# Kernel optimization log

Measured on AMD Instinct MI355X. Metric: run time of the kernel, lower is better.

The kernel has to match this reference:

```python
import jax, jax.numpy as jnp
import numpy as np

N_NODES = 50000
N_EDGES = 800000
NODE_DIM = 128
EDGE_DIM = 64
HIDDEN = 128
OUT_DIM = 64


def graph_conv(x, W, b, src, dst, num_segments):
    # h = linear(x); out[dst] += h[src]  (scatter-add / segment-sum aggregation)
    h = x @ W + b
    return jax.ops.segment_sum(h[src], dst, num_segments=num_segments)


def setup_inputs() -> dict:
    key = jax.random.key(0)
    ks = jax.random.split(key, 12)
    s = 1.0 / np.sqrt(HIDDEN)
    return {
        "node_features": jax.random.normal(ks[0], (N_NODES, NODE_DIM), dtype=jnp.float32),
        "edge_index": jax.random.randint(ks[1], (2, N_EDGES), 0, N_NODES, dtype=jnp.int64),
        "edge_features": jax.random.normal(ks[2], (N_EDGES, EDGE_DIM), dtype=jnp.float32),
        "edge_meta_index": jax.random.randint(ks[3], (2, N_EDGES), 0, N_EDGES, dtype=jnp.int64),
        "W1": jax.random.normal(ks[4], (NODE_DIM, HIDDEN), dtype=jnp.float32) * s,
        "b1": jnp.zeros((HIDDEN,), dtype=jnp.float32),
        "W2": jax.random.normal(ks[5], (HIDDEN, HIDDEN), dtype=jnp.float32) * s,
        "b2": jnp.zeros((HIDDEN,), dtype=jnp.float32),
        "We": jax.random.normal(ks[6], (EDGE_DIM, HIDDEN), dtype=jnp.float32) * s,
        "be": jnp.zeros((HIDDEN,), dtype=jnp.float32),
        "Wfc": jax.random.normal(ks[7], (2 * HIDDEN, OUT_DIM), dtype=jnp.float32) * s,
        "bfc": jnp.zeros((OUT_DIM,), dtype=jnp.float32),
    }


def reference(node_features, edge_index, edge_features, edge_meta_index,
              W1, b1, W2, b2, We, be, Wfc, bfc):
    row, col = edge_index[0], edge_index[1]
    mrow, mcol = edge_meta_index[0], edge_meta_index[1]

    # two node GraphConvs (dropout is identity in eval / p=0)
    x = jax.nn.relu(graph_conv(node_features, W1, b1, row, col, N_NODES))
    x = jax.nn.relu(graph_conv(x, W2, b2, row, col, N_NODES))

    # edge GraphConv on the line graph: e has one row per original edge
    e = graph_conv(edge_features, We, be, mrow, mcol, N_EDGES)

    # per-edge scatter-add aggregation (vectorized form of the Python loop):
    # aggregated_neighbors[dest] += x[src]; aggregated_edges[dest] += e[idx]
    agg_neighbors = jax.ops.segment_sum(x[row], col, num_segments=N_NODES)
    agg_edges = jax.ops.segment_sum(e, col, num_segments=N_NODES)

    out = jnp.concatenate([x + agg_neighbors, agg_edges], axis=1) @ Wfc + bfc
    return out
```

## Files before the change

kernel.cpp:

```cpp
#include <hip/hip_runtime.h>

#define N_NODES 50000
#define N_EDGES 800000
#define NODE_DIM 128
#define EDGE_DIM 64
#define HIDDEN 128
#define OUT_DIM 64

#define NBKT 196
#define CAP 4864
#define EPB 4096
#define NBLK1 196

typedef unsigned short u16;
typedef unsigned int u32;
typedef __attribute__((ext_vector_type(8))) short bf16x8;
typedef __attribute__((ext_vector_type(4))) float f32x4;

__device__ __forceinline__ float bflo(u32 u) { return __builtin_bit_cast(float, u << 16); }
__device__ __forceinline__ float bfhi(u32 u) { return __builtin_bit_cast(float, u & 0xFFFF0000u); }
__device__ __forceinline__ u32 pack2(float x, float y) {
    u32 a = __builtin_bit_cast(u32, x);
    a += 0x7FFFu + ((a >> 16) & 1u);
    u32 b = __builtin_bit_cast(u32, y);
    b += 0x7FFFu + ((b >> 16) & 1u);
    return (a >> 16) | (b & 0xFFFF0000u);
}
__device__ __forceinline__ u16 bf16r(float x) {
    u32 a = __builtin_bit_cast(u32, x);
    a += 0x7FFFu + ((a >> 16) & 1u);
    return (u16)(a >> 16);
}

__global__ __launch_bounds__(256) void pre1(
    const float* __restrict__ We, const float* __restrict__ be,
    const float* __restrict__ Wfc, const float* __restrict__ W1,
    const float* __restrict__ W2,
    float* __restrict__ Wcomb, float* __restrict__ bvec,
    short* __restrict__ W1t, short* __restrict__ W2t,
    int* __restrict__ bcur, int* __restrict__ bcurm)
{
    int idx = blockIdx.x * 256 + threadIdx.x;
    if (idx < 4096) {
        int k = idx >> 6, c = idx & 63;
        float s = 0.f;
        for (int h = 0; h < 128; h++)
            s = fmaf(We[k * 128 + h], Wfc[(128 + h) * 64 + c], s);
        Wcomb[idx] = s;
    } else if (idx < 4160) {
        int c = idx - 4096;
        float s = 0.f;
        for (int h = 0; h < 128; h++)
            s = fmaf(be[h], Wfc[(128 + h) * 64 + c], s);
        bvec[c] = s;
    } else if (idx < 20544) {
        int i = idx - 4160; int n = i >> 7, k = i & 127;
        W1t[n * 128 + k] = (short)bf16r(W1[k * 128 + n]);
    } else if (idx < 36928) {
        int i = idx - 20544; int n = i >> 7, k = i & 127;
        W2t[n * 128 + k] = (short)bf16r(W2[k * 128 + n]);
    } else if (idx < 37320) {
        int i = idx - 36928;
        if (i < 196) bcur[i] = i * CAP;
        else bcurm[i - 196] = (i - 196) * CAP;
    }
}

__global__ __launch_bounds__(256) void pre2(
    const float* __restrict__ Wfc, const float* __restrict__ Wcomb,
    short* __restrict__ Wft)
{
    int idx = blockIdx.x * 256 + threadIdx.x;
    if (idx < 64 * 192) {
        int n = idx / 192, k = idx - n * 192;
        float v = (k < 128) ? Wfc[k * 64 + n] : Wcomb[(k - 128) * 64 + n];
        Wft[n * 192 + k] = (short)bf16r(v);
    }
}

__global__ __launch_bounds__(256) void bin_pairs(
    const int* __restrict__ row, const int* __restrict__ col,
    const int* __restrict__ mrow, const int* __restrict__ mcol,
    int* __restrict__ bcur, int* __restrict__ bcurm,
    u32* __restrict__ pairs, u32* __restrict__ pairsm)
{
    int prob = (blockIdx.x >= NBLK1) ? 1 : 0;
    int blk = blockIdx.x - prob * NBLK1;
    int base = blk * EPB;
    int t = threadIdx.x;
    __shared__ int lh[NBKT];
    __shared__ int lbase[NBKT];
    __shared__ int lcur[NBKT];
    for (int i = t; i < NBKT; i += 256) { lh[i] = 0; lcur[i] = 0; }
    __syncthreads();
    int k[16], v[16];
    #pragma unroll
    for (int i = 0; i < 16; i++) {
        int idx = base + i * 256 + t;
        if (idx < N_EDGES) {
            if (!prob) { k[i] = col[idx]; v[i] = row[idx]; }
            else       { k[i] = col[mcol[idx]]; v[i] = mrow[idx]; }
            atomicAdd(&lh[k[i] >> 8], 1);
        } else {
            k[i] = -1; v[i] = 0;
        }
    }
    __syncthreads();
    int* gcur = prob ? bcurm : bcur;
    for (int i = t; i < NBKT; i += 256)
        lbase[i] = atomicAdd(&gcur[i], lh[i]);
    __syncthreads();
    u32* PR = prob ? pairsm : pairs;
    #pragma unroll
    for (int i = 0; i < 16; i++) {
        if (k[i] >= 0) {
            int bk = k[i] >> 8;
            int p = lbase[bk] + atomicAdd(&lcur[bk], 1);
            if (p < (bk + 1) * CAP)
                PR[p] = (u32)v[i] | ((u32)(k[i] & 255) << 24);
        }
    }
}

__global__ __launch_bounds__(256) void bucket_fill(
    const u32* __restrict__ pairs, const u32* __restrict__ pairsm,
    const int* __restrict__ bcur, const int* __restrict__ bcurm,
    int* __restrict__ offp, int* __restrict__ deg, int* __restrict__ ids,
    int* __restrict__ offpm, int* __restrict__ degm, int* __restrict__ idsm)
{
    int prob = (blockIdx.x >= NBKT) ? 1 : 0;
    int b = blockIdx.x - prob * NBKT;
    const u32* PR = prob ? pairsm : pairs;
    int cnt_total = (prob ? bcurm[b] : bcur[b]) - b * CAP;
    if (cnt_total > CAP) cnt_total = CAP;
    int n0 = b << 8;
    int nn = N_NODES - n0; if (nn > 256) nn = 256;
    __shared__ int hist[256];
    __shared__ int cur[256];
    __shared__ int wsum[4];
    __shared__ u32 pbuf[CAP];
    int t = threadIdx.x;
    hist[t] = 0;
    __syncthreads();
    for (int i = t; i < cnt_total; i += 256) {
        u32 pr = PR[(size_t)b * CAP + i];
        pbuf[i] = pr;
        atomicAdd(&hist[pr >> 24], 1);
    }
    __syncthreads();
    int h = hist[t];
    int x = h;
    int lane = t & 63, wid = t >> 6;
    for (int d = 1; d < 64; d <<= 1) {
        int u = __shfl_up(x, d, 64);
        if (lane >= d) x += u;
    }
    if (lane == 63) wsum[wid] = x;
    __syncthreads();
    int wex = 0;
    for (int i = 0; i < wid; i++) wex += wsum[i];
    int excl = wex + x - h;
    cur[t] = excl;
    if (t < nn) {
        if (!prob) { offp[n0 + t] = b * CAP + excl; deg[n0 + t] = h; }
        else       { offpm[n0 + t] = b * CAP + excl; degm[n0 + t] = h; }
    }
    __syncthreads();
    int* OI = prob ? idsm : ids;
    for (int i = t; i < cnt_total; i += 256) {
        u32 pr = pbuf[i];
        int p = atomicAdd(&cur[pr >> 24], 1);
        OI[(size_t)b * CAP + p] = (int)(pr & 0xFFFFFFu);
    }
}

__global__ __launch_bounds__(256) void gemm_mfma_f32(
    const float* __restrict__ A, const short* __restrict__ Wt,
    u16* __restrict__ P, int M)
{
    __shared__ short As[64 * 128];
    __shared__ short Ws[128 * 128];
    int t = threadIdx.x;
    int r0 = blockIdx.x * 64;
    for (int i = t; i < 64 * 32; i += 256) {
        int row = i >> 5, c4 = i & 31;
        int gr = r0 + row;
        float4 v = make_float4(0.f, 0.f, 0.f, 0.f);
        if (gr < M) v = ((const float4*)(A + (size_t)gr * 128))[c4];
        uint2 u; u.x = pack2(v.x, v.y); u.y = pack2(v.z, v.w);
        *(uint2*)((char*)As + row * 256 + ((c4 * 8) ^ ((row & 7) << 4))) = u;
    }
    for (int i = t; i < 128 * 16; i += 256) {
        int row = i >> 4, c16 = i & 15;
        uint4 u = *(const uint4*)((const char*)Wt + row * 256 + c16 * 16);
        *(uint4*)((char*)Ws + row * 256 + ((c16 * 16) ^ ((row & 7) << 4))) = u;
    }
    __syncthreads();
    int w = t >> 6, l = t & 63, lr = l & 15, q = l >> 4;
    int rh = (w & 1) * 32, ch = (w >> 1) * 64;
    f32x4 acc[2][4];
    #pragma unroll
    for (int rt = 0; rt < 2; rt++)
        #pragma unroll
        for (int ct = 0; ct < 4; ct++) acc[rt][ct] = (f32x4){0.f, 0.f, 0.f, 0.f};
    #pragma unroll
    for (int kk = 0; kk < 4; kk++) {
        int bo = kk * 64 + q * 16;
        bf16x8 a[2];
        #pragma unroll
        for (int rt = 0; rt < 2; rt++) {
            int ar = rh + rt * 16 + lr;
            a[rt] = *(const bf16x8*)((const char*)As + ar * 256 + (bo ^ ((ar & 7) << 4)));
        }
        #pragma unroll
        for (int ct = 0; ct < 4; ct++) {
            int br = ch + ct * 16 + lr;
            bf16x8 b = *(const bf16x8*)((const char*)Ws + br * 256 + (bo ^ ((br & 7) << 4)));
            acc[0][ct] = __builtin_amdgcn_mfma_f32_16x16x32_bf16(a[0], b, acc[0][ct], 0, 0, 0);
            acc[1][ct] = __builtin_amdgcn_mfma_f32_16x16x32_bf16(a[1], b, acc[1][ct], 0, 0, 0);
        }
    }
    #pragma unroll
    for (int rt = 0; rt < 2; rt++)
        #pragma unroll
        for (int reg = 0; reg < 4; reg++) {
            int gr = r0 + rh + rt * 16 + q * 4 + reg;
            if (gr < M) {
                #pragma unroll
                for (int ct = 0; ct < 4; ct++)
                    P[(size_t)gr * 128 + ch + ct * 16 + lr] = bf16r(acc[rt][ct][reg]);
            }
        }
}

__global__ __launch_bounds__(256) void gemm_mfma_bf16(
    const u16* __restrict__ A, const short* __restrict__ Wt,
    u16* __restrict__ P, int M)
{
    __shared__ short As[64 * 128];
    __shared__ short Ws[128 * 128];
    int t = threadIdx.x;
    int r0 = blockIdx.x * 64;
    for (int i = t; i < 64 * 16; i += 256) {
        int row = i >> 4, c16 = i & 15;
        int gr = r0 + row;
        uint4 u = make_uint4(0u, 0u, 0u, 0u);
        if (gr < M) u = *(const uint4*)((const char*)A + (size_t)gr * 256 + c16 * 16);
        *(uint4*)((char*)As + row * 256 + ((c16 * 16) ^ ((row & 7) << 4))) = u;
    }
    for (int i = t; i < 128 * 16; i += 256) {
        int row = i >> 4, c16 = i & 15;
        uint4 u = *(const uint4*)((const char*)Wt + row * 256 + c16 * 16);
        *(uint4*)((char*)Ws + row * 256 + ((c16 * 16) ^ ((row & 7) << 4))) = u;
    }
    __syncthreads();
    int w = t >> 6, l = t & 63, lr = l & 15, q = l >> 4;
    int rh = (w & 1) * 32, ch = (w >> 1) * 64;
    f32x4 acc[2][4];
    #pragma unroll
    for (int rt = 0; rt < 2; rt++)
        #pragma unroll
        for (int ct = 0; ct < 4; ct++) acc[rt][ct] = (f32x4){0.f, 0.f, 0.f, 0.f};
    #pragma unroll
    for (int kk = 0; kk < 4; kk++) {
        int bo = kk * 64 + q * 16;
        bf16x8 a[2];
        #pragma unroll
        for (int rt = 0; rt < 2; rt++) {
            int ar = rh + rt * 16 + lr;
            a[rt] = *(const bf16x8*)((const char*)As + ar * 256 + (bo ^ ((ar & 7) << 4)));
        }
        #pragma unroll
        for (int ct = 0; ct < 4; ct++) {
            int br = ch + ct * 16 + lr;
            bf16x8 b = *(const bf16x8*)((const char*)Ws + br * 256 + (bo ^ ((br & 7) << 4)));
            acc[0][ct] = __builtin_amdgcn_mfma_f32_16x16x32_bf16(a[0], b, acc[0][ct], 0, 0, 0);
            acc[1][ct] = __builtin_amdgcn_mfma_f32_16x16x32_bf16(a[1], b, acc[1][ct], 0, 0, 0);
        }
    }
    #pragma unroll
    for (int rt = 0; rt < 2; rt++)
        #pragma unroll
        for (int reg = 0; reg < 4; reg++) {
            int gr = r0 + rh + rt * 16 + q * 4 + reg;
            if (gr < M) {
                #pragma unroll
                for (int ct = 0; ct < 4; ct++)
                    P[(size_t)gr * 128 + ch + ct * 16 + lr] = bf16r(acc[rt][ct][reg]);
            }
        }
}

__global__ __launch_bounds__(256) void agg_relu_q(
    const u16* __restrict__ P, const int* __restrict__ offp,
    const int* __restrict__ deg,
    const int* __restrict__ ids, const float* __restrict__ bias,
    u16* __restrict__ X, int M)
{
    int qid = threadIdx.x >> 4;
    int l = threadIdx.x & 15;
    int w = blockIdx.x * 16 + qid;
    if (w >= M) return;
    int beg = offp[w], end = beg + deg[w];
    const uint4* F = (const uint4*)P;
    float a0 = 0.f, a1 = 0.f, a2 = 0.f, a3 = 0.f,
          a4 = 0.f, a5 = 0.f, a6 = 0.f, a7 = 0.f;
    int i = beg;
    for (; i + 3 < end; i += 4) {
        uint4 v0 = F[(size_t)ids[i]     * 16 + l];
        uint4 v1 = F[(size_t)ids[i + 1] * 16 + l];
        uint4 v2 = F[(size_t)ids[i + 2] * 16 + l];
        uint4 v3 = F[(size_t)ids[i + 3] * 16 + l];
        a0 += bflo(v0.x) + bflo(v1.x) + bflo(v2.x) + bflo(v3.x);
        a1 += bfhi(v0.x) + bfhi(v1.x) + bfhi(v2.x) + bfhi(v3.x);
        a2 += bflo(v0.y) + bflo(v1.y) + bflo(v2.y) + bflo(v3.y);
        a3 += bfhi(v0.y) + bfhi(v1.y) + bfhi(v2.y) + bfhi(v3.y);
        a4 += bflo(v0.z) + bflo(v1.z) + bflo(v2.z) + bflo(v3.z);
        a5 += bfhi(v0.z) + bfhi(v1.z) + bfhi(v2.z) + bfhi(v3.z);
        a6 += bflo(v0.w) + bflo(v1.w) + bflo(v2.w) + bflo(v3.w);
        a7 += bfhi(v0.w) + bfhi(v1.w) + bfhi(v2.w) + bfhi(v3.w);
    }
    for (; i < end; i++) {
        uint4 v = F[(size_t)ids[i] * 16 + l];
        a0 += bflo(v.x); a1 += bfhi(v.x);
        a2 += bflo(v.y); a3 += bfhi(v.y);
        a4 += bflo(v.z); a5 += bfhi(v.z);
        a6 += bflo(v.w); a7 += bfhi(v.w);
    }
    float dg = (float)(end - beg);
    float4 b0 = ((const float4*)bias)[2 * l];
    float4 b1 = ((const float4*)bias)[2 * l + 1];
    a0 = fmaxf(fmaf(dg, b0.x, a0), 0.f);
    a1 = fmaxf(fmaf(dg, b0.y, a1), 0.f);
    a2 = fmaxf(fmaf(dg, b0.z, a2), 0.f);
    a3 = fmaxf(fmaf(dg, b0.w, a3), 0.f);
    a4 = fmaxf(fmaf(dg, b1.x, a4), 0.f);
    a5 = fmaxf(fmaf(dg, b1.y, a5), 0.f);
    a6 = fmaxf(fmaf(dg, b1.z, a6), 0.f);
    a7 = fmaxf(fmaf(dg, b1.w, a7), 0.f);
    uint4 o;
    o.x = pack2(a0, a1); o.y = pack2(a2, a3);
    o.z = pack2(a4, a5); o.w = pack2(a6, a7);
    ((uint4*)(X + (size_t)w * 128))[l] = o;
}

__global__ __launch_bounds__(256) void agg_epilogue_q(
    const u16* __restrict__ X2, const float* __restrict__ ef,
    const int* __restrict__ offp, const int* __restrict__ deg,
    const int* __restrict__ ids,
    const int* __restrict__ offpm, const int* __restrict__ degm,
    const int* __restrict__ mids,
    u16* __restrict__ S, u16* __restrict__ Gg, int M)
{
    int qid = threadIdx.x >> 4;
    int l = threadIdx.x & 15;
    int w = blockIdx.x * 16 + qid;
    if (w >= M) return;
    {
        int beg = offp[w], end = beg + deg[w];
        const uint4* F = (const uint4*)X2;
        uint4 own = F[(size_t)w * 16 + l];
        float a0 = bflo(own.x), a1 = bfhi(own.x),
              a2 = bflo(own.y), a3 = bfhi(own.y),
              a4 = bflo(own.z), a5 = bfhi(own.z),
              a6 = bflo(own.w), a7 = bfhi(own.w);
        int i = beg;
        for (; i + 3 < end; i += 4) {
            uint4 v0 = F[(size_t)ids[i]     * 16 + l];
            uint4 v1 = F[(size_t)ids[i + 1] * 16 + l];
            uint4 v2 = F[(size_t)ids[i + 2] * 16 + l];
            uint4 v3 = F[(size_t)ids[i + 3] * 16 + l];
            a0 += bflo(v0.x) + bflo(v1.x) + bflo(v2.x) + bflo(v3.x);
            a1 += bfhi(v0.x) + bfhi(v1.x) + bfhi(v2.x) + bfhi(v3.x);
            a2 += bflo(v0.y) + bflo(v1.y) + bflo(v2.y) + bflo(v3.y);
            a3 += bfhi(v0.y) + bfhi(v1.y) + bfhi(v2.y) + bfhi(v3.y);
            a4 += bflo(v0.z) + bflo(v1.z) + bflo(v2.z) + bflo(v3.z);
            a5 += bfhi(v0.z) + bfhi(v1.z) + bfhi(v2.z) + bfhi(v3.z);
            a6 += bflo(v0.w) + bflo(v1.w) + bflo(v2.w) + bflo(v3.w);
            a7 += bfhi(v0.w) + bfhi(v1.w) + bfhi(v2.w) + bfhi(v3.w);
        }
        for (; i < end; i++) {
            uint4 v = F[(size_t)ids[i] * 16 + l];
            a0 += bflo(v.x); a1 += bfhi(v.x);
            a2 += bflo(v.y); a3 += bfhi(v.y);
            a4 += bflo(v.z); a5 += bfhi(v.z);
            a6 += bflo(v.w); a7 += bfhi(v.w);
        }
        uint4 o;
        o.x = pack2(a0, a1); o.y = pack2(a2, a3);
        o.z = pack2(a4, a5); o.w = pack2(a6, a7);
        ((uint4*)(S + (size_t)w * 128))[l] = o;
    }
    {
        int beg = offpm[w], end = beg + degm[w];
        const float4* E = (const float4*)ef;
        float g0 = 0.f, g1 = 0.f, g2 = 0.f, g3 = 0.f;
        int i = beg;
        for (; i + 3 < end; i += 4) {
            float4 v0 = E[(size_t)mids[i]     * 16 + l];
            float4 v1 = E[(size_t)mids[i + 1] * 16 + l];
            float4 v2 = E[(size_t)mids[i + 2] * 16 + l];
            float4 v3 = E[(size_t)mids[i + 3] * 16 + l];
            g0 += v0.x + v1.x + v2.x + v3.x;
            g1 += v0.y + v1.y + v2.y + v3.y;
            g2 += v0.z + v1.z + v2.z + v3.z;
            g3 += v0.w + v1.w + v2.w + v3.w;
        }
        for (; i < end; i++) {
            float4 v = E[(size_t)mids[i] * 16 + l];
            g0 += v.x; g1 += v.y; g2 += v.z; g3 += v.w;
        }
        uint2 o;
        o.x = pack2(g0, g1); o.y = pack2(g2, g3);
        ((uint2*)(Gg + (size_t)w * 64))[l] = o;
    }
}

__global__ __launch_bounds__(256) void final_mfma(
    const u16* __restrict__ S, const u16* __restrict__ Gg,
    const int* __restrict__ degm, const short* __restrict__ Wft,
    const float* __restrict__ bvec, const float* __restrict__ bfc,
    float* __restrict__ out, int M)
{
    __shared__ short As[64 * 192];
    __shared__ short Ws[64 * 192];
    int t = threadIdx.x;
    int r0 = blockIdx.x * 64;
    for (int i = t; i < 64 * 16; i += 256) {
        int row = i >> 4, c16 = i & 15;
        int gr = r0 + row;
        uint4 u = make_uint4(0u, 0u, 0u, 0u);
        if (gr < M) u = *(const uint4*)((const char*)S + (size_t)gr * 256 + c16 * 16);
        *(uint4*)((char*)As + row * 384 + ((c16 * 16) ^ ((row & 7) << 4))) = u;
    }
    for (int i = t; i < 64 * 8; i += 256) {
        int row = i >> 3, c16 = i & 7;
        int gr = r0 + row;
        uint4 u = make_uint4(0u, 0u, 0u, 0u);
        if (gr < M) u = *(const uint4*)((const char*)Gg + (size_t)gr * 128 + c16 * 16);
        *(uint4*)((char*)As + row * 384 + ((256 + c16 * 16) ^ ((row & 7) << 4))) = u;
    }
    for (int i = t; i < 64 * 24; i += 256) {
        int row = i / 24, c16 = i - row * 24;
        uint4 u = *(const uint4*)((const char*)Wft + row * 384 + c16 * 16);
        *(uint4*)((char*)Ws + row * 384 + ((c16 * 16) ^ ((row & 7) << 4))) = u;
    }
    __syncthreads();
    int w = t >> 6, l = t & 63, lr = l & 15, q = l >> 4;
    int rh = (w & 1) * 32, ch = (w >> 1) * 32;
    f32x4 acc[2][2];
    #pragma unroll
    for (int rt = 0; rt < 2; rt++)
        #pragma unroll
        for (int ct = 0; ct < 2; ct++) acc[rt][ct] = (f32x4){0.f, 0.f, 0.f, 0.f};
    #pragma unroll
    for (int kk = 0; kk < 6; kk++) {
        int bo = kk * 64 + q * 16;
        bf16x8 a[2];
        #pragma unroll
        for (int rt = 0; rt < 2; rt++) {
            int ar = rh + rt * 16 + lr;
            a[rt] = *(const bf16x8*)((const char*)As + ar * 384 + (bo ^ ((ar & 7) << 4)));
        }
        #pragma unroll
        for (int ct = 0; ct < 2; ct++) {
            int br = ch + ct * 16 + lr;
            bf16x8 b = *(const bf16x8*)((const char*)Ws + br * 384 + (bo ^ ((br & 7) << 4)));
            acc[0][ct] = __builtin_amdgcn_mfma_f32_16x16x32_bf16(a[0], b, acc[0][ct], 0, 0, 0);
            acc[1][ct] = __builtin_amdgcn_mfma_f32_16x16x32_bf16(a[1], b, acc[1][ct], 0, 0, 0);
        }
    }
    float bv0 = bvec[ch + lr], bv1 = bvec[ch + 16 + lr];
    float bf0 = bfc[ch + lr],  bf1 = bfc[ch + 16 + lr];
    #pragma unroll
    for (int rt = 0; rt < 2; rt++)
        #pragma unroll
        for (int reg = 0; reg < 4; reg++) {
            int gr = r0 + rh + rt * 16 + q * 4 + reg;
            if (gr < M) {
                float cnt = (float)degm[gr];
                out[(size_t)gr * 64 + ch + lr]      = acc[rt][0][reg] + fmaf(cnt, bv0, bf0);
                out[(size_t)gr * 64 + ch + 16 + lr] = acc[rt][1][reg] + fmaf(cnt, bv1, bf1);
            }
        }
}

extern "C" void kernel_launch(void* const* d_in, const int* in_sizes, int n_in,
                              void* d_out, int out_size, void* d_ws, size_t ws_size,
                              hipStream_t stream)
{
    const float* nf  = (const float*)d_in[0];
    const int*   ei  = (const int*)d_in[1];
    const float* ef  = (const float*)d_in[2];
    const int*   emi = (const int*)d_in[3];
    const float* W1  = (const float*)d_in[4];
    const float* b1  = (const float*)d_in[5];
    const float* W2  = (const float*)d_in[6];
    const float* b2  = (const float*)d_in[7];
    const float* We  = (const float*)d_in[8];
    const float* be  = (const float*)d_in[9];
    const float* Wfc = (const float*)d_in[10];
    const float* bfc = (const float*)d_in[11];

    const int* row  = ei;
    const int* col  = ei + N_EDGES;
    const int* mrow = emi;
    const int* mcol = emi + N_EDGES;

    u16* A  = (u16*)d_ws;
    u16* B  = A + (size_t)N_NODES * 128;
    u16* S  = B + (size_t)N_NODES * 128;
    u16* Gg = S + (size_t)N_NODES * 128;
    u32* pairs  = (u32*)(Gg + (size_t)N_NODES * 64);
    u32* pairsm = pairs + (size_t)NBKT * CAP;
    float* Wcomb = (float*)(pairsm + (size_t)NBKT * CAP);
    float* bvec  = Wcomb + 64 * 64;
    short* W1t = (short*)(bvec + 64);
    short* W2t = W1t + 128 * 128;
    short* Wft = W2t + 128 * 128;
    int* offp  = (int*)(Wft + 64 * 192);
    int* deg   = offp + N_NODES;
    int* offpm = deg + N_NODES;
    int* degm  = offpm + N_NODES;
    int* bcur  = degm + N_NODES;
    int* bcurm = bcur + 256;
    int* ids   = bcurm + 256;
    int* idsm  = ids + (size_t)NBKT * CAP;

    pre1<<<146, 256, 0, stream>>>(We, be, Wfc, W1, W2, Wcomb, bvec, W1t, W2t, bcur, bcurm);

    bin_pairs<<<2 * NBLK1, 256, 0, stream>>>(row, col, mrow, mcol,
                                             bcur, bcurm, pairs, pairsm);
    bucket_fill<<<2 * NBKT, 256, 0, stream>>>(pairs, pairsm, bcur, bcurm,
                                              offp, deg, ids, offpm, degm, idsm);
    pre2<<<48, 256, 0, stream>>>(Wfc, Wcomb, Wft);

    gemm_mfma_f32<<<(N_NODES + 63) / 64, 256, 0, stream>>>(nf, W1t, A, N_NODES);
    agg_relu_q<<<(N_NODES + 15) / 16, 256, 0, stream>>>(A, offp, deg, ids, b1, B, N_NODES);
    gemm_mfma_bf16<<<(N_NODES + 63) / 64, 256, 0, stream>>>(B, W2t, A, N_NODES);
    agg_relu_q<<<(N_NODES + 15) / 16, 256, 0, stream>>>(A, offp, deg, ids, b2, B, N_NODES);
    agg_epilogue_q<<<(N_NODES + 15) / 16, 256, 0, stream>>>(
        B, ef, offp, deg, ids, offpm, degm, idsm, S, Gg, N_NODES);
    final_mfma<<<(N_NODES + 63) / 64, 256, 0, stream>>>(
        S, Gg, degm, Wft, bvec, bfc, (float*)d_out, N_NODES);
}
```

Baseline: 482.1 us.

## Split node features into column slices for cache-resident gathers

```diff
diff --git a/kernel.cpp b/kernel.cpp
--- a/kernel.cpp
+++ b/kernel.cpp
@@ -11,6 +11,10 @@
 #define CAP 4864
 #define EPB 4096
 #define NBLK1 196
+
+#define NSLC 4
+#define SLC_STRIDE ((size_t)N_NODES * 32)
+#define NBN 782
 
 typedef unsigned short u16;
 typedef unsigned int u32;
@@ -227,8 +231,11 @@
             int gr = r0 + rh + rt * 16 + q * 4 + reg;
             if (gr < M) {
                 #pragma unroll
-                for (int ct = 0; ct < 4; ct++)
-                    P[(size_t)gr * 128 + ch + ct * 16 + lr] = bf16r(acc[rt][ct][reg]);
+                for (int ct = 0; ct < 4; ct++) {
+                    int cb = ch + ct * 16;
+                    P[(size_t)(cb >> 5) * SLC_STRIDE + (size_t)gr * 32 + (cb & 31) + lr]
+                        = bf16r(acc[rt][ct][reg]);
+                }
             }
         }
 }
@@ -245,7 +252,8 @@
         int row = i >> 4, c16 = i & 15;
         int gr = r0 + row;
         uint4 u = make_uint4(0u, 0u, 0u, 0u);
-        if (gr < M) u = *(const uint4*)((const char*)A + (size_t)gr * 256 + c16 * 16);
+        if (gr < M)
+            u = ((const uint4*)(A + (size_t)(c16 >> 2) * SLC_STRIDE + (size_t)gr * 32))[c16 & 3];
         *(uint4*)((char*)As + row * 256 + ((c16 * 16) ^ ((row & 7) << 4))) = u;
     }
     for (int i = t; i < 128 * 16; i += 256) {
@@ -285,32 +293,37 @@
             int gr = r0 + rh + rt * 16 + q * 4 + reg;
             if (gr < M) {
                 #pragma unroll
-                for (int ct = 0; ct < 4; ct++)
-                    P[(size_t)gr * 128 + ch + ct * 16 + lr] = bf16r(acc[rt][ct][reg]);
+                for (int ct = 0; ct < 4; ct++) {
+                    int cb = ch + ct * 16;
+                    P[(size_t)(cb >> 5) * SLC_STRIDE + (size_t)gr * 32 + (cb & 31) + lr]
+                        = bf16r(acc[rt][ct][reg]);
+                }
             }
         }
 }
 
-__global__ __launch_bounds__(256) void agg_relu_q(
+__global__ __launch_bounds__(256) void agg_relu_s(
     const u16* __restrict__ P, const int* __restrict__ offp,
     const int* __restrict__ deg,
     const int* __restrict__ ids, const float* __restrict__ bias,
     u16* __restrict__ X, int M)
 {
-    int qid = threadIdx.x >> 4;
-    int l = threadIdx.x & 15;
-    int w = blockIdx.x * 16 + qid;
+    int s  = blockIdx.x / NBN;
+    int nb = blockIdx.x - s * NBN;
+    int g  = threadIdx.x >> 2;
+    int l4 = threadIdx.x & 3;
+    int w = nb * 64 + g;
     if (w >= M) return;
     int beg = offp[w], end = beg + deg[w];
-    const uint4* F = (const uint4*)P;
+    const uint4* F = (const uint4*)(P + (size_t)s * SLC_STRIDE);
     float a0 = 0.f, a1 = 0.f, a2 = 0.f, a3 = 0.f,
           a4 = 0.f, a5 = 0.f, a6 = 0.f, a7 = 0.f;
     int i = beg;
     for (; i + 3 < end; i += 4) {
-        uint4 v0 = F[(size_t)ids[i]     * 16 + l];
-        uint4 v1 = F[(size_t)ids[i + 1] * 16 + l];
-        uint4 v2 = F[(size_t)ids[i + 2] * 16 + l];
-        uint4 v3 = F[(size_t)ids[i + 3] * 16 + l];
+        uint4 v0 = F[(size_t)ids[i]     * 4 + l4];
+        uint4 v1 = F[(size_t)ids[i + 1] * 4 + l4];
+        uint4 v2 = F[(size_t)ids[i + 2] * 4 + l4];
+        uint4 v3 = F[(size_t)ids[i + 3] * 4 + l4];
         a0 += bflo(v0.x) + bflo(v1.x) + bflo(v2.x) + bflo(v3.x);
         a1 += bfhi(v0.x) + bfhi(v1.x) + bfhi(v2.x) + bfhi(v3.x);
         a2 += bflo(v0.y) + bflo(v1.y) + bflo(v2.y) + bflo(v3.y);
@@ -321,15 +334,16 @@
         a7 += bfhi(v0.w) + bfhi(v1.w) + bfhi(v2.w) + bfhi(v3.w);
     }
     for (; i < end; i++) {
-        uint4 v = F[(size_t)ids[i] * 16 + l];
+        uint4 v = F[(size_t)ids[i] * 4 + l4];
         a0 += bflo(v.x); a1 += bfhi(v.x);
         a2 += bflo(v.y); a3 += bfhi(v.y);
         a4 += bflo(v.z); a5 += bfhi(v.z);
         a6 += bflo(v.w); a7 += bfhi(v.w);
     }
     float dg = (float)(end - beg);
-    float4 b0 = ((const float4*)bias)[2 * l];
-    float4 b1 = ((const float4*)bias)[2 * l + 1];
+    const float4* Bv = (const float4*)(bias + s * 32);
+    float4 b0 = Bv[l4 * 2];
+    float4 b1 = Bv[l4 * 2 + 1];
     a0 = fmaxf(fmaf(dg, b0.x, a0), 0.f);
     a1 = fmaxf(fmaf(dg, b0.y, a1), 0.f);
     a2 = fmaxf(fmaf(dg, b0.z, a2), 0.f);
@@ -341,79 +355,86 @@
     uint4 o;
     o.x = pack2(a0, a1); o.y = pack2(a2, a3);
     o.z = pack2(a4, a5); o.w = pack2(a6, a7);
-    ((uint4*)(X + (size_t)w * 128))[l] = o;
-}
-
-__global__ __launch_bounds__(256) void agg_epilogue_q(
-    const u16* __restrict__ X2, const float* __restrict__ ef,
-    const int* __restrict__ offp, const int* __restrict__ deg,
-    const int* __restrict__ ids,
+    ((uint4*)(X + (size_t)s * SLC_STRIDE + (size_t)w * 32))[l4] = o;
+}
+
+__global__ __launch_bounds__(256) void agg_s_epi(
+    const u16* __restrict__ X2, const int* __restrict__ offp,
+    const int* __restrict__ deg, const int* __restrict__ ids,
+    u16* __restrict__ S, int M)
+{
+    int s  = blockIdx.x / NBN;
+    int nb = blockIdx.x - s * NBN;
+    int g  = threadIdx.x >> 2;
+    int l4 = threadIdx.x & 3;
+    int w = nb * 64 + g;
+    if (w >= M) return;
+    int beg = offp[w], end = beg + deg[w];
+    const uint4* F = (const uint4*)(X2 + (size_t)s * SLC_STRIDE);
+    uint4 own = F[(size_t)w * 4 + l4];
+    float a0 = bflo(own.x), a1 = bfhi(own.x),
+          a2 = bflo(own.y), a3 = bfhi(own.y),
+          a4 = bflo(own.z), a5 = bfhi(own.z),
+          a6 = bflo(own.w), a7 = bfhi(own.w);
+    int i = beg;
+    for (; i + 3 < end; i += 4) {
+        uint4 v0 = F[(size_t)ids[i]     * 4 + l4];
+        uint4 v1 = F[(size_t)ids[i + 1] * 4 + l4];
+        uint4 v2 = F[(size_t)ids[i + 2] * 4 + l4];
+        uint4 v3 = F[(size_t)ids[i + 3] * 4 + l4];
+        a0 += bflo(v0.x) + bflo(v1.x) + bflo(v2.x) + bflo(v3.x);
+        a1 += bfhi(v0.x) + bfhi(v1.x) + bfhi(v2.x) + bfhi(v3.x);
+        a2 += bflo(v0.y) + bflo(v1.y) + bflo(v2.y) + bflo(v3.y);
+        a3 += bfhi(v0.y) + bfhi(v1.y) + bfhi(v2.y) + bfhi(v3.y);
+        a4 += bflo(v0.z) + bflo(v1.z) + bflo(v2.z) + bflo(v3.z);
+        a5 += bfhi(v0.z) + bfhi(v1.z) + bfhi(v2.z) + bfhi(v3.z);
+        a6 += bflo(v0.w) + bflo(v1.w) + bflo(v2.w) + bflo(v3.w);
+        a7 += bfhi(v0.w) + bfhi(v1.w) + bfhi(v2.w) + bfhi(v3.w);
+    }
+    for (; i < end; i++) {
+        uint4 v = F[(size_t)ids[i] * 4 + l4];
+        a0 += bflo(v.x); a1 += bfhi(v.x);
+        a2 += bflo(v.y); a3 += bfhi(v.y);
+        a4 += bflo(v.z); a5 += bfhi(v.z);
+        a6 += bflo(v.w); a7 += bfhi(v.w);
+    }
+    uint4 o;
+    o.x = pack2(a0, a1); o.y = pack2(a2, a3);
+    o.z = pack2(a4, a5); o.w = pack2(a6, a7);
+    ((uint4*)(S + (size_t)w * 128))[s * 4 + l4] = o;
+}
+
+__global__ __launch_bounds__(256) void agg_meta_q(
+    const float* __restrict__ ef,
     const int* __restrict__ offpm, const int* __restrict__ degm,
     const int* __restrict__ mids,
-    u16* __restrict__ S, u16* __restrict__ Gg, int M)
+    u16* __restrict__ Gg, int M)
 {
     int qid = threadIdx.x >> 4;
     int l = threadIdx.x & 15;
     int w = blockIdx.x * 16 + qid;
     if (w >= M) return;
-    {
-        int beg = offp[w], end = beg + deg[w];
-        const uint4* F = (const uint4*)X2;
-        uint4 own = F[(size_t)w * 16 + l];
-        float a0 = bflo(own.x), a1 = bfhi(own.x),
-              a2 = bflo(own.y), a3 = bfhi(own.y),
-              a4 = bflo(own.z), a5 = bfhi(own.z),
-              a6 = bflo(own.w), a7 = bfhi(own.w);
-        int i = beg;
-        for (; i + 3 < end; i += 4) {
-            uint4 v0 = F[(size_t)ids[i]     * 16 + l];
-            uint4 v1 = F[(size_t)ids[i + 1] * 16 + l];
-            uint4 v2 = F[(size_t)ids[i + 2] * 16 + l];
-            uint4 v3 = F[(size_t)ids[i + 3] * 16 + l];
-            a0 += bflo(v0.x) + bflo(v1.x) + bflo(v2.x) + bflo(v3.x);
-            a1 += bfhi(v0.x) + bfhi(v1.x) + bfhi(v2.x) + bfhi(v3.x);
-            a2 += bflo(v0.y) + bflo(v1.y) + bflo(v2.y) + bflo(v3.y);
-            a3 += bfhi(v0.y) + bfhi(v1.y) + bfhi(v2.y) + bfhi(v3.y);
-            a4 += bflo(v0.z) + bflo(v1.z) + bflo(v2.z) + bflo(v3.z);
-            a5 += bfhi(v0.z) + bfhi(v1.z) + bfhi(v2.z) + bfhi(v3.z);
-            a6 += bflo(v0.w) + bflo(v1.w) + bflo(v2.w) + bflo(v3.w);
-            a7 += bfhi(v0.w) + bfhi(v1.w) + bfhi(v2.w) + bfhi(v3.w);
-        }
-        for (; i < end; i++) {
-            uint4 v = F[(size_t)ids[i] * 16 + l];
-            a0 += bflo(v.x); a1 += bfhi(v.x);
-            a2 += bflo(v.y); a3 += bfhi(v.y);
-            a4 += bflo(v.z); a5 += bfhi(v.z);
-            a6 += bflo(v.w); a7 += bfhi(v.w);
-        }
-        uint4 o;
-        o.x = pack2(a0, a1); o.y = pack2(a2, a3);
-        o.z = pack2(a4, a5); o.w = pack2(a6, a7);
-        ((uint4*)(S + (size_t)w * 128))[l] = o;
-    }
-    {
-        int beg = offpm[w], end = beg + degm[w];
-        const float4* E = (const float4*)ef;
-        float g0 = 0.f, g1 = 0.f, g2 = 0.f, g3 = 0.f;
-        int i = beg;
-        for (; i + 3 < end; i += 4) {
-            float4 v0 = E[(size_t)mids[i]     * 16 + l];
-            float4 v1 = E[(size_t)mids[i + 1] * 16 + l];
-            float4 v2 = E[(size_t)mids[i + 2] * 16 + l];
-            float4 v3 = E[(size_t)mids[i + 3] * 16 + l];
-            g0 += v0.x + v1.x + v2.x + v3.x;
-            g1 += v0.y + v1.y + v2.y + v3.y;
-            g2 += v0.z + v1.z + v2.z + v3.z;
-            g3 += v0.w + v1.w + v2.w + v3.w;
-        }
-        for (; i < end; i++) {
-            float4 v = E[(size_t)mids[i] * 16 + l];
-            g0 += v.x; g1 += v.y; g2 += v.z; g3 += v.w;
-        }
-        uint2 o;
-        o.x = pack2(g0, g1); o.y = pack2(g2, g3);
-        ((uint2*)(Gg + (size_t)w * 64))[l] = o;
-    }
+    int beg = offpm[w], end = beg + degm[w];
+    const float4* E = (const float4*)ef;
+    float g0 = 0.f, g1 = 0.f, g2 = 0.f, g3 = 0.f;
+    int i = beg;
+    for (; i + 3 < end; i += 4) {
+        float4 v0 = E[(size_t)mids[i]     * 16 + l];
+        float4 v1 = E[(size_t)mids[i + 1] * 16 + l];
+        float4 v2 = E[(size_t)mids[i + 2] * 16 + l];
+        float4 v3 = E[(size_t)mids[i + 3] * 16 + l];
+        g0 += v0.x + v1.x + v2.x + v3.x;
+        g1 += v0.y + v1.y + v2.y + v3.y;
+        g2 += v0.z + v1.z + v2.z + v3.z;
+        g3 += v0.w + v1.w + v2.w + v3.w;
+    }
+    for (; i < end; i++) {
+        float4 v = E[(size_t)mids[i] * 16 + l];
+        g0 += v.x; g1 += v.y; g2 += v.z; g3 += v.w;
+    }
+    uint2 o;
+    o.x = pack2(g0, g1); o.y = pack2(g2, g3);
+    ((uint2*)(Gg + (size_t)w * 64))[l] = o;
 }
 
 __global__ __launch_bounds__(256) void final_mfma(
@@ -536,11 +557,11 @@
     pre2<<<48, 256, 0, stream>>>(Wfc, Wcomb, Wft);
 
     gemm_mfma_f32<<<(N_NODES + 63) / 64, 256, 0, stream>>>(nf, W1t, A, N_NODES);
-    agg_relu_q<<<(N_NODES + 15) / 16, 256, 0, stream>>>(A, offp, deg, ids, b1, B, N_NODES);
+    agg_relu_s<<<NSLC * NBN, 256, 0, stream>>>(A, offp, deg, ids, b1, B, N_NODES);
     gemm_mfma_bf16<<<(N_NODES + 63) / 64, 256, 0, stream>>>(B, W2t, A, N_NODES);
-    agg_relu_q<<<(N_NODES + 15) / 16, 256, 0, stream>>>(A, offp, deg, ids, b2, B, N_NODES);
-    agg_epilogue_q<<<(N_NODES + 15) / 16, 256, 0, stream>>>(
-        B, ef, offp, deg, ids, offpm, degm, idsm, S, Gg, N_NODES);
+    agg_relu_s<<<NSLC * NBN, 256, 0, stream>>>(A, offp, deg, ids, b2, B, N_NODES);
+    agg_s_epi<<<NSLC * NBN, 256, 0, stream>>>(B, offp, deg, ids, S, N_NODES);
+    agg_meta_q<<<(N_NODES + 15) / 16, 256, 0, stream>>>(ef, offpm, degm, idsm, Gg, N_NODES);
     final_mfma<<<(N_NODES + 63) / 64, 256, 0, stream>>>(
         S, Gg, degm, Wft, bvec, bfc, (float*)d_out, N_NODES);
 }
```

New measurement: 521.0 us. 1.08x slower.
